# Performance work log

Hardware: AMD Instinct MI355X
Metric: run time of the kernel (lower is better)

## Reference

```python
import jax, jax.numpy as jnp
import numpy as np

B, T, E, D, H = 32, 2048, 512, 1024, 128

def setup_inputs() -> dict:
    key = jax.random.key(0)
    ks = jax.random.split(key, 8)
    encoder_outs = jax.random.normal(ks[0], (B, T, E), dtype=jnp.float32)
    decoder_state = jax.random.normal(ks[1], (B, D), dtype=jnp.float32)
    # valid lengths in [T//2, T]; mask=True on padded positions
    src_lens = jnp.clip(jax.random.randint(ks[2], (B,), 0, T), T // 2, T).astype(jnp.int32)
    mask = jnp.arange(T)[None, :] >= src_lens[:, None]  # [B,T] bool
    # parameters (nn.Linear style: y = x @ W^T + b; here stored pre-transposed)
    W_enc = jax.random.normal(ks[3], (E, H), dtype=jnp.float32) / np.sqrt(E)
    b_enc = jnp.zeros((H,), dtype=jnp.float32)
    W_dec = jax.random.normal(ks[4], (D, H), dtype=jnp.float32) / np.sqrt(D)  # bias=False
    w_w = jax.random.normal(ks[5], (H, 1), dtype=jnp.float32) / np.sqrt(H)
    w_b = jnp.zeros((1,), dtype=jnp.float32)
    return {"encoder_outs": encoder_outs, "src_lens": src_lens, "decoder_state": decoder_state,
            "mask": mask, "W_enc": W_enc, "b_enc": b_enc, "W_dec": W_dec, "w_w": w_w, "w_b": w_b}

def reference(encoder_outs, src_lens, decoder_state, mask, W_enc, b_enc, W_dec, w_w, w_b):
    # processed_memory = mlp_enc(encoder_outs): [B,T,H]
    processed = jnp.einsum('bte,eh->bth', encoder_outs, W_enc) + b_enc
    # mlp_dec(decoder_state).unsqueeze(1): [B,1,H]
    dec = (decoder_state @ W_dec)[:, None, :]
    # erg = w(tanh(processed + dec)).squeeze(-1): [B,T]
    erg = jnp.einsum('bth,h->bt', jnp.tanh(processed + dec), w_w[:, 0]) + w_b[0]
    erg = jnp.where(mask, -jnp.inf, erg)
    attention_weights = jax.nn.softmax(erg, axis=1)  # [B,T]
    attention_context = jnp.einsum('bte,bt->be', encoder_outs, attention_weights)  # [B,E]
    return attention_context, attention_weights
```

## Files before the change

### kernel.cpp

```cpp
#include <hip/hip_runtime.h>
#include <hip/hip_bf16.h>

#define B 32
#define T 2048
#define E 512
#define D 1024
#define H 128

typedef __attribute__((ext_vector_type(8))) short bf16x8;
typedef __attribute__((ext_vector_type(4))) float f32x4;

static __device__ __forceinline__ short f2b(float f) {
  __hip_bfloat16 h = __float2bfloat16(f);
  return __builtin_bit_cast(short, h);
}

__global__ __launch_bounds__(512) void prep_kernel(
    const float* __restrict__ ds, const float* __restrict__ Wd,
    const float* __restrict__ be, const float* __restrict__ We,
    float* __restrict__ dec_ws, char* __restrict__ WeT) {
  const int tid = threadIdx.x;
  if (blockIdx.x < 32) {
    const int b = blockIdx.x;
    const int h = tid & 127;
    const int kg = tid >> 7;
    __shared__ float sds[D];
    __shared__ float sred[4][H];
    for (int i = tid; i < D; i += 512) sds[i] = ds[b * D + i];
    __syncthreads();
    float acc = 0.0f;
    const int k0 = kg * 256;
#pragma unroll 8
    for (int k = k0; k < k0 + 256; ++k) acc = fmaf(sds[k], Wd[k * H + h], acc);
    sred[kg][h] = acc;
    __syncthreads();
    if (kg == 0)
      dec_ws[b * H + h] = be[h] + sred[0][h] + sred[1][h] + sred[2][h] + sred[3][h];
  } else {
    const int id = (blockIdx.x - 32) * 512 + tid;
    const int c = id >> 10;
    const int rem = id & 1023;
    const int h = rem & 127;
    const int s = rem >> 7;
    const int k0 = c * 64 + s * 8;
    bf16x8 v;
#pragma unroll
    for (int j = 0; j < 8; ++j) v[j] = f2b(We[(k0 + j) * H + h]);
    *(bf16x8*)(WeT + c * 16384 + h * 128 + ((s ^ (h & 7)) * 16)) = v;
  }
}

__global__ __launch_bounds__(1024, 1) void erg_mfma_kernel(
    const float* __restrict__ enc, const char* __restrict__ WeT,
    const float* __restrict__ dec_ws, const float* __restrict__ ww,
    const float* __restrict__ wb, float* __restrict__ erg_ws) {
  __shared__ __align__(16) char smem[131072];
  const int tid = threadIdx.x;
  const int lane = tid & 63;
  const int w = tid >> 6;
  const int m = lane & 15;
  const int g = lane >> 4;
  const int row0 = blockIdx.x * 256 + w * 16;
  const int b = row0 >> 11;

#pragma unroll
  for (int j = 0; j < 8; ++j)
    __builtin_amdgcn_global_load_lds(
        (const __attribute__((address_space(1))) void*)(WeT + j * 16384 + tid * 16),
        (__attribute__((address_space(3))) void*)(&smem[j * 16384 + tid * 16]),
        16, 0, 0);

  f32x4 acc[8];
#pragma unroll
  for (int n = 0; n < 8; ++n) {
    const float d = dec_ws[b * H + n * 16 + m];
    acc[n] = (f32x4){d, d, d, d};
  }

  const float* arow = enc + (size_t)(row0 + m) * E + g * 8;

  float4 a0 = *(const float4*)(arow);
  float4 a1 = *(const float4*)(arow + 4);
  float4 a2 = *(const float4*)(arow + 32);
  float4 a3 = *(const float4*)(arow + 36);

  asm volatile("s_waitcnt vmcnt(0)" ::: "memory");
  __syncthreads();

#pragma unroll
  for (int c = 0; c < 8; ++c) {
    float4 n0, n1, n2, n3;
    if (c < 7) {
      const float* ak = arow + (c + 1) * 64;
      n0 = *(const float4*)(ak);
      n1 = *(const float4*)(ak + 4);
      n2 = *(const float4*)(ak + 32);
      n3 = *(const float4*)(ak + 36);
    }
    bf16x8 af0, af1;
    af0[0] = f2b(a0.x); af0[1] = f2b(a0.y); af0[2] = f2b(a0.z); af0[3] = f2b(a0.w);
    af0[4] = f2b(a1.x); af0[5] = f2b(a1.y); af0[6] = f2b(a1.z); af0[7] = f2b(a1.w);
    af1[0] = f2b(a2.x); af1[1] = f2b(a2.y); af1[2] = f2b(a2.z); af1[3] = f2b(a2.w);
    af1[4] = f2b(a3.x); af1[5] = f2b(a3.y); af1[6] = f2b(a3.z); af1[7] = f2b(a3.w);

#pragma unroll
    for (int kk = 0; kk < 2; ++kk) {
      const int slot = (((kk * 4) + g) ^ (m & 7)) * 16;
      const bf16x8 af = kk ? af1 : af0;
#pragma unroll
      for (int n = 0; n < 8; ++n) {
        const bf16x8 bf =
            *(const bf16x8*)(&smem[c * 16384 + (n * 16 + m) * 128 + slot]);
        acc[n] = __builtin_amdgcn_mfma_f32_16x16x32_bf16(af, bf, acc[n], 0, 0, 0);
      }
    }
    a0 = n0; a1 = n1; a2 = n2; a3 = n3;
  }

  const float wbv = wb[0];
  float wwreg[8];
#pragma unroll
  for (int n = 0; n < 8; ++n) wwreg[n] = ww[n * 16 + m];
#pragma unroll
  for (int j = 0; j < 4; ++j) {
    float gsum = 0.0f;
#pragma unroll
    for (int n = 0; n < 8; ++n) {
      const float x = acc[n][j];
      const float th = 1.0f - 2.0f / (__expf(2.0f * x) + 1.0f);
      gsum = fmaf(wwreg[n], th, gsum);
    }
#pragma unroll
    for (int off = 1; off < 16; off <<= 1) gsum += __shfl_xor(gsum, off, 64);
    if (m == 0) erg_ws[row0 + g * 4 + j] = gsum + wbv;
  }
}

__global__ __launch_bounds__(256) void softmax_kernel(
    const float* __restrict__ erg_ws, const int* __restrict__ src_lens,
    float* __restrict__ wout) {
  const int b = blockIdx.x;
  const int n = src_lens[b];
  const int tid = threadIdx.x;
  const int lane = tid & 63, wid = tid >> 6;
  __shared__ float sm[4];

  float v[T / 256];
  float mx = -1e30f;
#pragma unroll
  for (int r = 0; r < T / 256; ++r) {
    const int t = tid + r * 256;
    const float x = erg_ws[b * T + t];
    v[r] = (t < n) ? x : -1e30f;
    mx = fmaxf(mx, v[r]);
  }
#pragma unroll
  for (int off = 32; off > 0; off >>= 1) mx = fmaxf(mx, __shfl_xor(mx, off, 64));
  if (lane == 0) sm[wid] = mx;
  __syncthreads();
  mx = fmaxf(fmaxf(sm[0], sm[1]), fmaxf(sm[2], sm[3]));
  __syncthreads();

  float s = 0.0f;
#pragma unroll
  for (int r = 0; r < T / 256; ++r) {
    const float e = (v[r] > -1e29f) ? __expf(v[r] - mx) : 0.0f;
    v[r] = e;
    s += e;
  }
#pragma unroll
  for (int off = 32; off > 0; off >>= 1) s += __shfl_xor(s, off, 64);
  if (lane == 0) sm[wid] = s;
  __syncthreads();
  s = sm[0] + sm[1] + sm[2] + sm[3];
  const float inv = 1.0f / s;
#pragma unroll
  for (int r = 0; r < T / 256; ++r) wout[b * T + tid + r * 256] = v[r] * inv;
}

__global__ __launch_bounds__(256) void ctxp_kernel(
    const float* __restrict__ enc, const float* __restrict__ w,
    float* __restrict__ part) {
  const int b = blockIdx.y;
  const int ch = blockIdx.x;
  const int e4 = threadIdx.x & 127;
  const int tp = threadIdx.x >> 7;
  __shared__ float sw[128];
  if (threadIdx.x < 128) sw[threadIdx.x] = w[b * T + ch * 128 + threadIdx.x];
  __syncthreads();
  const float4* ep = (const float4*)(enc + ((size_t)b * T + ch * 128) * E) + e4;
  float4 acc = {0.0f, 0.0f, 0.0f, 0.0f};
#pragma unroll 8
  for (int t = tp; t < 128; t += 2) {
    const float4 e = ep[(size_t)t * (E / 4)];
    const float wv = sw[t];
    acc.x = fmaf(e.x, wv, acc.x);
    acc.y = fmaf(e.y, wv, acc.y);
    acc.z = fmaf(e.z, wv, acc.z);
    acc.w = fmaf(e.w, wv, acc.w);
  }
  *(float4*)(part + ((size_t)(b * 32 + ch * 2 + tp)) * E + e4 * 4) = acc;
}

__global__ __launch_bounds__(128) void ctxr_kernel(
    const float* __restrict__ part, float* __restrict__ ctx) {
  const int b = blockIdx.x;
  const int e4 = threadIdx.x;
  float4 acc = {0.0f, 0.0f, 0.0f, 0.0f};
#pragma unroll
  for (int p = 0; p < 32; ++p) {
    const float4 v = *(const float4*)(part + ((size_t)(b * 32 + p)) * E + e4 * 4);
    acc.x += v.x; acc.y += v.y; acc.z += v.z; acc.w += v.w;
  }
  *(float4*)(ctx + b * E + e4 * 4) = acc;
}

extern "C" void kernel_launch(void* const* d_in, const int* in_sizes, int n_in,
                              void* d_out, int out_size, void* d_ws,
                              size_t ws_size, hipStream_t stream) {
  const float* enc = (const float*)d_in[0];
  const int* src_lens = (const int*)d_in[1];
  const float* ds = (const float*)d_in[2];
  const float* We = (const float*)d_in[4];
  const float* be = (const float*)d_in[5];
  const float* Wd = (const float*)d_in[6];
  const float* ww = (const float*)d_in[7];
  const float* wb = (const float*)d_in[8];

  float* ctx_out = (float*)d_out;
  float* w_out = (float*)d_out + B * E;

  float* ws = (float*)d_ws;
  float* dec_ws = ws;
  float* erg_ws = ws + B * H;
  char* WeT = (char*)(ws + B * H + B * T);
  float* part = ws + B * H + B * T + 32768;

  prep_kernel<<<48, 512, 0, stream>>>(ds, Wd, be, We, dec_ws, WeT);
  erg_mfma_kernel<<<(B * T) / 256, 1024, 0, stream>>>(enc, WeT, dec_ws, ww, wb, erg_ws);
  softmax_kernel<<<B, 256, 0, stream>>>(erg_ws, src_lens, w_out);
  ctxp_kernel<<<dim3(16, B), 256, 0, stream>>>(enc, w_out, part);
  ctxr_kernel<<<B, 128, 0, stream>>>(part, ctx_out);
}
```

Measured before the change: 257.5 us.

## Fuse softmax and context reduction into one per-batch kernel

Merges the softmax, partial-context and context-reduce kernels into a single kernel with one 1024-thread block per batch row. Weights are kept in shared memory and the per-batch context is reduced in LDS, removing the partial-sum workspace and two launches. In exchange, the bandwidth-heavy pass over encoder outputs now runs on only 32 blocks, which may underuse the GPU's memory bandwidth.

```diff
diff --git a/kernel.cpp b/kernel.cpp
--- a/kernel.cpp
+++ b/kernel.cpp
@@ -136,83 +136,84 @@
   }
 }
 
-__global__ __launch_bounds__(256) void softmax_kernel(
-    const float* __restrict__ erg_ws, const int* __restrict__ src_lens,
-    float* __restrict__ wout) {
+__global__ __launch_bounds__(1024, 1) void softmax_ctx_kernel(
+    const float* __restrict__ enc, const float* __restrict__ erg_ws,
+    const int* __restrict__ src_lens, float* __restrict__ w_out,
+    float* __restrict__ ctx) {
   const int b = blockIdx.x;
+  const int tid = threadIdx.x;
+  const int lane = tid & 63, w = tid >> 6;
   const int n = src_lens[b];
-  const int tid = threadIdx.x;
-  const int lane = tid & 63, wid = tid >> 6;
-  __shared__ float sm[4];
-
-  float v[T / 256];
-  float mx = -1e30f;
-#pragma unroll
-  for (int r = 0; r < T / 256; ++r) {
-    const int t = tid + r * 256;
-    const float x = erg_ws[b * T + t];
-    v[r] = (t < n) ? x : -1e30f;
-    mx = fmaxf(mx, v[r]);
-  }
+
+  __shared__ float sw[T];
+  __shared__ float red8[8][E];
+  __shared__ float sred[16];
+  __shared__ float sscal[2];
+
+  const float x0 = erg_ws[b * T + tid];
+  const float x1 = erg_ws[b * T + tid + 1024];
+  const float v0 = (tid < n) ? x0 : -1e30f;
+  const float v1 = (tid + 1024 < n) ? x1 : -1e30f;
+
+  float mx = fmaxf(v0, v1);
 #pragma unroll
   for (int off = 32; off > 0; off >>= 1) mx = fmaxf(mx, __shfl_xor(mx, off, 64));
-  if (lane == 0) sm[wid] = mx;
-  __syncthreads();
-  mx = fmaxf(fmaxf(sm[0], sm[1]), fmaxf(sm[2], sm[3]));
-  __syncthreads();
-
-  float s = 0.0f;
-#pragma unroll
-  for (int r = 0; r < T / 256; ++r) {
-    const float e = (v[r] > -1e29f) ? __expf(v[r] - mx) : 0.0f;
-    v[r] = e;
-    s += e;
-  }
+  if (lane == 0) sred[w] = mx;
+  __syncthreads();
+  if (tid == 0) {
+    float m2 = sred[0];
+#pragma unroll
+    for (int i = 1; i < 16; ++i) m2 = fmaxf(m2, sred[i]);
+    sscal[0] = m2;
+  }
+  __syncthreads();
+  mx = sscal[0];
+
+  const float e0 = (v0 > -1e29f) ? __expf(v0 - mx) : 0.0f;
+  const float e1 = (v1 > -1e29f) ? __expf(v1 - mx) : 0.0f;
+  float s = e0 + e1;
 #pragma unroll
   for (int off = 32; off > 0; off >>= 1) s += __shfl_xor(s, off, 64);
-  if (lane == 0) sm[wid] = s;
-  __syncthreads();
-  s = sm[0] + sm[1] + sm[2] + sm[3];
-  const float inv = 1.0f / s;
-#pragma unroll
-  for (int r = 0; r < T / 256; ++r) wout[b * T + tid + r * 256] = v[r] * inv;
-}
-
-__global__ __launch_bounds__(256) void ctxp_kernel(
-    const float* __restrict__ enc, const float* __restrict__ w,
-    float* __restrict__ part) {
-  const int b = blockIdx.y;
-  const int ch = blockIdx.x;
-  const int e4 = threadIdx.x & 127;
-  const int tp = threadIdx.x >> 7;
-  __shared__ float sw[128];
-  if (threadIdx.x < 128) sw[threadIdx.x] = w[b * T + ch * 128 + threadIdx.x];
-  __syncthreads();
-  const float4* ep = (const float4*)(enc + ((size_t)b * T + ch * 128) * E) + e4;
+  if (lane == 0) sred[w] = s;
+  __syncthreads();
+  if (tid == 0) {
+    float ss = 0.0f;
+#pragma unroll
+    for (int i = 0; i < 16; ++i) ss += sred[i];
+    sscal[1] = 1.0f / ss;
+  }
+  __syncthreads();
+  const float inv = sscal[1];
+
+  const float w0 = e0 * inv, w1 = e1 * inv;
+  w_out[b * T + tid] = w0;
+  w_out[b * T + tid + 1024] = w1;
+  sw[tid] = w0;
+  sw[tid + 1024] = w1;
+  __syncthreads();
+
+  const int e4 = tid & 127;
+  const int tg = tid >> 7;
+  const float4* ep = (const float4*)(enc + ((size_t)b * T + tg * 256) * E) + e4;
+  const float* swp = &sw[tg * 256];
   float4 acc = {0.0f, 0.0f, 0.0f, 0.0f};
 #pragma unroll 8
-  for (int t = tp; t < 128; t += 2) {
-    const float4 e = ep[(size_t)t * (E / 4)];
-    const float wv = sw[t];
+  for (int i = 0; i < 256; ++i) {
+    const float4 e = ep[(size_t)i * (E / 4)];
+    const float wv = swp[i];
     acc.x = fmaf(e.x, wv, acc.x);
     acc.y = fmaf(e.y, wv, acc.y);
     acc.z = fmaf(e.z, wv, acc.z);
     acc.w = fmaf(e.w, wv, acc.w);
   }
-  *(float4*)(part + ((size_t)(b * 32 + ch * 2 + tp)) * E + e4 * 4) = acc;
-}
-
-__global__ __launch_bounds__(128) void ctxr_kernel(
-    const float* __restrict__ part, float* __restrict__ ctx) {
-  const int b = blockIdx.x;
-  const int e4 = threadIdx.x;
-  float4 acc = {0.0f, 0.0f, 0.0f, 0.0f};
-#pragma unroll
-  for (int p = 0; p < 32; ++p) {
-    const float4 v = *(const float4*)(part + ((size_t)(b * 32 + p)) * E + e4 * 4);
-    acc.x += v.x; acc.y += v.y; acc.z += v.z; acc.w += v.w;
-  }
-  *(float4*)(ctx + b * E + e4 * 4) = acc;
+  *(float4*)&red8[tg][e4 * 4] = acc;
+  __syncthreads();
+  if (tid < E) {
+    float r = 0.0f;
+#pragma unroll
+    for (int p = 0; p < 8; ++p) r += red8[p][tid];
+    ctx[b * E + tid] = r;
+  }
 }
 
 extern "C" void kernel_launch(void* const* d_in, const int* in_sizes, int n_in,
@@ -234,11 +235,8 @@
   float* dec_ws = ws;
   float* erg_ws = ws + B * H;
   char* WeT = (char*)(ws + B * H + B * T);
-  float* part = ws + B * H + B * T + 32768;
 
   prep_kernel<<<48, 512, 0, stream>>>(ds, Wd, be, We, dec_ws, WeT);
   erg_mfma_kernel<<<(B * T) / 256, 1024, 0, stream>>>(enc, WeT, dec_ws, ww, wb, erg_ws);
-  softmax_kernel<<<B, 256, 0, stream>>>(erg_ws, src_lens, w_out);
-  ctxp_kernel<<<dim3(16, B), 256, 0, stream>>>(enc, w_out, part);
-  ctxr_kernel<<<B, 128, 0, stream>>>(part, ctx_out);
-}
+  softmax_ctx_kernel<<<B, 1024, 0, stream>>>(enc, erg_ws, src_lens, w_out, ctx_out);
+}
```

Measured after the change: 273.2 us. 6.1% more time.
